# Kernel tuning notes

Measured on AMD Instinct MI355X. Metric: run time of the kernel, lower is better.

The kernel has to match this reference:

```python
import jax, jax.numpy as jnp
import numpy as np


def euler_xyz_to_matrix(angles):
    # pytorch3d euler_angles_to_matrix(angles, 'XYZ') = R_X(a0) @ R_Y(a1) @ R_Z(a2)
    ax, ay, az = angles[..., 0], angles[..., 1], angles[..., 2]
    cx, sx = jnp.cos(ax), jnp.sin(ax)
    cy, sy = jnp.cos(ay), jnp.sin(ay)
    cz, sz = jnp.cos(az), jnp.sin(az)
    one = jnp.ones_like(ax)
    zero = jnp.zeros_like(ax)
    Rx = jnp.stack([one, zero, zero, zero, cx, -sx, zero, sx, cx], axis=-1).reshape(*ax.shape, 3, 3)
    Ry = jnp.stack([cy, zero, sy, zero, one, zero, -sy, zero, cy], axis=-1).reshape(*ax.shape, 3, 3)
    Rz = jnp.stack([cz, -sz, zero, sz, cz, zero, zero, zero, one], axis=-1).reshape(*ax.shape, 3, 3)
    return Rx @ Ry @ Rz


def chamfer_bidir(x, y):
    # x, y: [R, I, N, 3]. Squared-distance chamfer, mean point reduction, per (R,I) batch.
    x2 = jnp.sum(x * x, axis=-1)  # [R,I,N]
    y2 = jnp.sum(y * y, axis=-1)  # [R,I,N]
    # d2[r,i,n,m] = |x_n - y_m|^2
    d2 = x2[..., :, None] + y2[..., None, :] - 2.0 * jnp.einsum('rind,rimd->rinm', x, y)
    cham_x = jnp.mean(jnp.min(d2, axis=-1), axis=-1)  # x -> nearest y
    cham_y = jnp.mean(jnp.min(d2, axis=-2), axis=-1)  # y -> nearest x
    return cham_x + cham_y  # [R, I]


def setup_inputs() -> dict:
    key = jax.random.key(0)
    k1, k2, k3, k4 = jax.random.split(key, 4)
    R, I, N = 4, 16, 2048
    source_points = jax.random.normal(k1, (R, I, N, 3), dtype=jnp.float32)
    target_points = jax.random.normal(k2, (I, N, 3), dtype=jnp.float32)
    rotation = 0.1 * jax.random.normal(k3, (R, I, 3), dtype=jnp.float32)
    translation = 0.1 * jax.random.normal(k4, (R, I, 3), dtype=jnp.float32)
    scale = jnp.ones((R, I), dtype=jnp.float32)
    return {
        'source_points': source_points,
        'target_points': target_points,
        'rotation': rotation,
        'translation': translation,
        'scale': scale,
    }


def reference(source_points, target_points, rotation, translation, scale):
    R, I, N, _ = source_points.shape
    rot = euler_xyz_to_matrix(rotation)  # [R,I,3,3]
    # Transform per original: 4x4 matrix with rows [:3,:] scaled by `scale`,
    # so p' = scale * (rot @ p + translation).
    transformed = scale[..., None, None] * (
        jnp.einsum('rind,rikd->rink', source_points, rot) + translation[..., None, :]
    )  # [R,I,N,3]
    # target_points [I,N,3] broadcast to [R,I,N,3] (original repeats along R)
    target = jnp.broadcast_to(target_points[None], transformed.shape)
    # original calls chamfer_distance(target, transformed): x=target, y=transformed
    return chamfer_bidir(target, transformed)  # [R, I]
```

## Files before the change

### kernel.cpp

```cpp
#include <hip/hip_runtime.h>
#include <math.h>

#define RDIM 4
#define IDIM 16
#define NPAIR 64
#define NPTS 2048
#define THREADS 256
#define ROWSB 256
#define RBLK (NPTS / ROWSB)
#define TILES (NPTS / 32)
#define PSPLIT 4
#define ONEBF 0x3F80u

typedef __attribute__((ext_vector_type(8))) short bf16x8;
typedef __attribute__((ext_vector_type(16))) float f32x16;
typedef __attribute__((ext_vector_type(4))) float f32x4;

__device__ __forceinline__ float min3f(float a, float b, float c) {
    return fminf(a, fminf(b, c));
}

__device__ __forceinline__ unsigned int fkey(float f) {
    const unsigned int u = __float_as_uint(f);
    return (u & 0x80000000u) ? ~u : (u | 0x80000000u);
}
__device__ __forceinline__ float funkey(unsigned int k) {
    const unsigned int u = (k & 0x80000000u) ? (k ^ 0x80000000u) : ~k;
    return __uint_as_float(u);
}

__device__ __forceinline__ unsigned int f2bf(float f) {
    union { float f; unsigned int u; } v; v.f = f;
    return (v.u + 0x7FFFu + ((v.u >> 16) & 1u)) >> 16;
}
__device__ __forceinline__ float bf2f(unsigned int h) {
    union { unsigned int u; float f; } v; v.u = h << 16; return v.f;
}

__device__ __forceinline__ void make_rot(const float* __restrict__ rotv, int pair,
                                         float& r00, float& r01, float& r02,
                                         float& r10, float& r11, float& r12,
                                         float& r20, float& r21, float& r22) {
    const float ax = rotv[pair * 3 + 0];
    const float ay = rotv[pair * 3 + 1];
    const float az = rotv[pair * 3 + 2];
    float sx, cx, sy, cy, sz, cz;
    sincosf(ax, &sx, &cx);
    sincosf(ay, &sy, &cy);
    sincosf(az, &sz, &cz);
    r00 = cy * cz;                r01 = -cy * sz;               r02 = sy;
    r10 = cx * sz + sx * sy * cz; r11 = cx * cz - sx * sy * sz; r12 = -sx * cy;
    r20 = sx * sz - cx * sy * cz; r21 = sx * cz + cx * sy * sz; r22 = cx * cy;
}

__device__ __forceinline__ uint4 brec(float v0, float v1, float v2) {
    const float b0 = -2.0f * v0, b1 = -2.0f * v1, b2 = -2.0f * v2;
    const unsigned int h0 = f2bf(b0), h1 = f2bf(b1), h2 = f2bf(b2);
    const unsigned int l0 = f2bf(b0 - bf2f(h0));
    const unsigned int l1 = f2bf(b1 - bf2f(h1));
    const unsigned int l2 = f2bf(b2 - bf2f(h2));
    const float n2 = v0 * v0 + v1 * v1 + v2 * v2;
    const unsigned int nh = f2bf(n2), nl = f2bf(n2 - bf2f(nh));
    return make_uint4(h0 | (h1 << 16), h2 | (l0 << 16), l1 | (l2 << 16), nh | (nl << 16));
}
__device__ __forceinline__ void arec(float q0, float q1, float q2, uint4& a0, uint4& a1) {
    const unsigned int h0 = f2bf(q0), h1 = f2bf(q1), h2 = f2bf(q2);
    const unsigned int l0 = f2bf(q0 - bf2f(h0));
    const unsigned int l1 = f2bf(q1 - bf2f(h1));
    const unsigned int l2 = f2bf(q2 - bf2f(h2));
    a0 = make_uint4(h0 | (h1 << 16), h2 | (l0 << 16), l1 | (l2 << 16), ONEBF);
    a1 = make_uint4(l0 | (l1 << 16), l2 | (h0 << 16), h1 | (h2 << 16), ONEBF << 16);
}

__global__ __launch_bounds__(THREADS)
void prep(const float* __restrict__ src, const float* __restrict__ tgt,
          const float* __restrict__ rotv, const float* __restrict__ trav,
          const float* __restrict__ scal,
          uint4* __restrict__ Yb, uint4* __restrict__ Xa,
          unsigned int* __restrict__ colminU,
          float* __restrict__ out)
{
    const int b   = blockIdx.x;
    const int seg = blockIdx.y;
    const int tid = threadIdx.x;
    if (b == 0 && seg == 0 && tid < NPAIR) out[tid] = 0.0f;
    const int m0  = seg * (NPTS / PSPLIT);
    if (b < NPAIR) {
        const int pair = b;
        colminU[(size_t)pair * NPTS + m0 + tid * 2 + 0] = 0xFFFFFFFFu;
        colminU[(size_t)pair * NPTS + m0 + tid * 2 + 1] = 0xFFFFFFFFu;
        float r00, r01, r02, r10, r11, r12, r20, r21, r22;
        make_rot(rotv, pair, r00, r01, r02, r10, r11, r12, r20, r21, r22);
        const float t0 = trav[pair * 3 + 0];
        const float t1 = trav[pair * 3 + 1];
        const float t2 = trav[pair * 3 + 2];
        const float s  = scal[pair];
        const float* __restrict__ srcp = src + (size_t)pair * NPTS * 3;
#pragma unroll
        for (int u = 0; u < NPTS / THREADS / PSPLIT; ++u) {
            const int m = m0 + u * THREADS + tid;
            const float p0 = srcp[m * 3 + 0];
            const float p1 = srcp[m * 3 + 1];
            const float p2 = srcp[m * 3 + 2];
            const float y0 = s * fmaf(r00, p0, fmaf(r01, p1, fmaf(r02, p2, t0)));
            const float y1 = s * fmaf(r10, p0, fmaf(r11, p1, fmaf(r12, p2, t1)));
            const float y2 = s * fmaf(r20, p0, fmaf(r21, p1, fmaf(r22, p2, t2)));
            Yb[(size_t)pair * NPTS + m] = brec(y0, y1, y2);
        }
    } else {
        const int i = b - NPAIR;
        const float* __restrict__ tgtp = tgt + (size_t)i * NPTS * 3;
#pragma unroll
        for (int u = 0; u < NPTS / THREADS / PSPLIT; ++u) {
            const int m = m0 + u * THREADS + tid;
            const float x0 = tgtp[m * 3 + 0];
            const float x1 = tgtp[m * 3 + 1];
            const float x2 = tgtp[m * 3 + 2];
            uint4 a0, a1;
            arec(x0, x1, x2, a0, a1);
            Xa[((size_t)i * NPTS + m) * 2 + 0] = a0;
            Xa[((size_t)i * NPTS + m) * 2 + 1] = a1;
        }
    }
}

__global__ __launch_bounds__(THREADS, 2)
void chamfer_main(const uint4* __restrict__ Yb, const uint4* __restrict__ Xa,
                  unsigned int* __restrict__ colminU,
                  float* __restrict__ out)
{
    __shared__ alignas(16) unsigned char smem[32768];
    __shared__ unsigned int colpartU[NPTS];
    __shared__ float sx[ROWSB];
    __shared__ float rowmin[ROWSB];
    __shared__ float wsum[4];
    unsigned short* sB = (unsigned short*)smem;

    const int pair  = blockIdx.x;
    const int rb    = blockIdx.y;
    const int i     = pair & (IDIM - 1);
    const int tid   = threadIdx.x;
    const int lane  = tid & 63;
    const int w     = tid >> 6;
    const int c31   = lane & 31;
    const int h     = lane >> 5;

    const uint4* __restrict__ gB = Yb + (size_t)pair * NPTS;
    const char* gAb = (const char*)(Xa + ((size_t)i * NPTS + rb * ROWSB) * 2);

#pragma unroll
    for (int j = 0; j < 8; ++j)
        ((uint4*)sB)[j * THREADS + tid] = gB[j * THREADS + tid];
#pragma unroll
    for (int k = 0; k < 8; ++k)
        colpartU[k * THREADS + tid] = 0xFFFFFFFFu;
    {
        const unsigned short* ar = (const unsigned short*)(gAb + tid * 32);
        const float q0 = bf2f(ar[0]) + bf2f(ar[3]);
        const float q1 = bf2f(ar[1]) + bf2f(ar[4]);
        const float q2 = bf2f(ar[2]) + bf2f(ar[5]);
        sx[tid] = q0 * q0 + q1 * q1 + q2 * q2;
    }

    const bf16x8 af0 = *(const bf16x8*)(gAb + (w * 64 + c31) * 32 + h * 16);
    const bf16x8 af1 = *(const bf16x8*)(gAb + (w * 64 + 32 + c31) * 32 + h * 16);

    __syncthreads();

    f32x16 cx0, cx1;
#pragma unroll
    for (int j = 0; j < 16; ++j) {
        const int r = (j & 3) + 8 * (j >> 2) + 4 * h;
        cx0[j] = sx[w * 64 + r];
        cx1[j] = sx[w * 64 + 32 + r];
    }

    float mn0[16], mn1[16];
#pragma unroll
    for (int j = 0; j < 16; ++j) { mn0[j] = 3.4e38f; mn1[j] = 3.4e38f; }

    bf16x8 bfA = *(const bf16x8*)&sB[(0 * 32 + c31) * 8];
    bf16x8 bfB = *(const bf16x8*)&sB[(1 * 32 + c31) * 8];
    for (int t = 0; t < TILES; t += 2) {
        const f32x16 a0 = __builtin_amdgcn_mfma_f32_32x32x16_bf16(af0, bfA, cx0, 0, 0, 0);
        const f32x16 a1 = __builtin_amdgcn_mfma_f32_32x32x16_bf16(af1, bfA, cx1, 0, 0, 0);
        const f32x16 b0 = __builtin_amdgcn_mfma_f32_32x32x16_bf16(af0, bfB, cx0, 0, 0, 0);
        const f32x16 b1 = __builtin_amdgcn_mfma_f32_32x32x16_bf16(af1, bfB, cx1, 0, 0, 0);
        bfA = *(const bf16x8*)&sB[((((t + 2) & 63)) * 32 + c31) * 8];
        bfB = *(const bf16x8*)&sB[((((t + 3) & 63)) * 32 + c31) * 8];
#pragma unroll
        for (int j = 0; j < 16; ++j) {
            mn0[j] = min3f(mn0[j], a0[j], b0[j]);
            mn1[j] = min3f(mn1[j], a1[j], b1[j]);
        }
        float ca = fminf(a0[0], a1[0]);
        float cb = fminf(b0[0], b1[0]);
#pragma unroll
        for (int j = 1; j < 16; ++j) {
            ca = min3f(ca, a0[j], a1[j]);
            cb = min3f(cb, b0[j], b1[j]);
        }
        ca = fminf(ca, __shfl_xor(ca, 32, 64));
        cb = fminf(cb, __shfl_xor(cb, 32, 64));
        if (h == 0) {
            atomicMin(&colpartU[(t + 0) * 32 + c31], fkey(ca));
            atomicMin(&colpartU[(t + 1) * 32 + c31], fkey(cb));
        }
    }
    __syncthreads();

#pragma unroll
    for (int j = 0; j < 16; ++j) {
        float v0 = mn0[j], v1 = mn1[j];
        v0 = fminf(v0, __shfl_xor(v0, 1, 64));
        v1 = fminf(v1, __shfl_xor(v1, 1, 64));
        v0 = fminf(v0, __shfl_xor(v0, 2, 64));
        v1 = fminf(v1, __shfl_xor(v1, 2, 64));
        v0 = fminf(v0, __shfl_xor(v0, 4, 64));
        v1 = fminf(v1, __shfl_xor(v1, 4, 64));
        v0 = fminf(v0, __shfl_xor(v0, 8, 64));
        v1 = fminf(v1, __shfl_xor(v1, 8, 64));
        v0 = fminf(v0, __shfl_xor(v0, 16, 64));
        v1 = fminf(v1, __shfl_xor(v1, 16, 64));
        mn0[j] = v0; mn1[j] = v1;
    }
    if (c31 == 0) {
#pragma unroll
        for (int g = 0; g < 4; ++g) {
            f32x4 v4, u4;
            v4[0] = mn0[g * 4 + 0]; v4[1] = mn0[g * 4 + 1];
            v4[2] = mn0[g * 4 + 2]; v4[3] = mn0[g * 4 + 3];
            u4[0] = mn1[g * 4 + 0]; u4[1] = mn1[g * 4 + 1];
            u4[2] = mn1[g * 4 + 2]; u4[3] = mn1[g * 4 + 3];
            *(f32x4*)&rowmin[w * 64 + 8 * g + 4 * h] = v4;
            *(f32x4*)&rowmin[w * 64 + 32 + 8 * g + 4 * h] = u4;
        }
    }

#pragma unroll
    for (int k = 0; k < 8; ++k) {
        const int col = k * THREADS + tid;
        atomicMin(&colminU[(size_t)pair * NPTS + col], colpartU[col]);
    }
    __syncthreads();

    float v = rowmin[tid];
#pragma unroll
    for (int off = 32; off > 0; off >>= 1)
        v += __shfl_down(v, off, 64);
    if (lane == 0) wsum[w] = v;
    __syncthreads();
    if (tid == 0) {
        const float tot = wsum[0] + wsum[1] + wsum[2] + wsum[3];
        atomicAdd(&out[pair], tot * (1.0f / NPTS));
    }
}

__global__ __launch_bounds__(THREADS)
void chamfer_col(const unsigned int* __restrict__ colminU, float* __restrict__ out)
{
    __shared__ float wsum[4];
    const int pair = blockIdx.x;
    const int tid  = threadIdx.x;
    const int lane = tid & 63;
    const int w    = tid >> 6;
    float s = 0.0f;
#pragma unroll
    for (int k = 0; k < 8; ++k) {
        const int col = k * THREADS + tid;
        s += funkey(colminU[(size_t)pair * NPTS + col]);
    }
#pragma unroll
    for (int off = 32; off > 0; off >>= 1)
        s += __shfl_down(s, off, 64);
    if (lane == 0) wsum[w] = s;
    __syncthreads();
    if (tid == 0) {
        const float tot = wsum[0] + wsum[1] + wsum[2] + wsum[3];
        atomicAdd(&out[pair], tot * (1.0f / NPTS));
    }
}

extern "C" void kernel_launch(void* const* d_in, const int* in_sizes, int n_in,
                              void* d_out, int out_size, void* d_ws, size_t ws_size,
                              hipStream_t stream) {
    const float* src  = (const float*)d_in[0];
    const float* tgt  = (const float*)d_in[1];
    const float* rotv = (const float*)d_in[2];
    const float* trav = (const float*)d_in[3];
    const float* scal = (const float*)d_in[4];
    float* out = (float*)d_out;

    char* ws = (char*)d_ws;
    uint4* Yb = (uint4*)ws;
    uint4* Xa = (uint4*)(ws + (size_t)NPAIR * NPTS * 16);
    unsigned int* colminU = (unsigned int*)(ws + (size_t)NPAIR * NPTS * 16
                                               + (size_t)IDIM * NPTS * 32);

    dim3 pgrid(NPAIR + IDIM, PSPLIT);
    prep<<<pgrid, THREADS, 0, stream>>>(src, tgt, rotv, trav, scal, Yb, Xa, colminU, out);

    dim3 grid(NPAIR, RBLK);
    chamfer_main<<<grid, THREADS, 0, stream>>>(Yb, Xa, colminU, out);

    chamfer_col<<<NPAIR, THREADS, 0, stream>>>(colminU, out);
}
```

Before: 95.12 us.

## Fuse point prep into main chamfer kernel and replace atomics with partial buffers

Removes the separate prep kernel. Each main block now transforms its pair's source points and encodes its own target rows straight into shared memory, and the target norms come from the split-bf16 encoding. Global atomicMin on column minima and atomicAdd on outputs are replaced by per-row-block partial key arrays, which the final kernel reduces with a min over row blocks. This saves one launch and the workspace round trip, and removes the need to initialise the output. In exchange, every row block redundantly recomputes the rotation and encoding for all 2048 source points, and more partial data is written and read back.

```diff
diff --git a/kernel.cpp b/kernel.cpp
--- a/kernel.cpp
+++ b/kernel.cpp
@@ -9,7 +9,6 @@
 #define ROWSB 256
 #define RBLK (NPTS / ROWSB)
 #define TILES (NPTS / 32)
-#define PSPLIT 4
 #define ONEBF 0x3F80u
 
 typedef __attribute__((ext_vector_type(8))) short bf16x8;
@@ -63,73 +62,29 @@
     const unsigned int nh = f2bf(n2), nl = f2bf(n2 - bf2f(nh));
     return make_uint4(h0 | (h1 << 16), h2 | (l0 << 16), l1 | (l2 << 16), nh | (nl << 16));
 }
-__device__ __forceinline__ void arec(float q0, float q1, float q2, uint4& a0, uint4& a1) {
+__device__ __forceinline__ void arec(float q0, float q1, float q2, uint4& a0, uint4& a1,
+                                     float& qn2) {
     const unsigned int h0 = f2bf(q0), h1 = f2bf(q1), h2 = f2bf(q2);
     const unsigned int l0 = f2bf(q0 - bf2f(h0));
     const unsigned int l1 = f2bf(q1 - bf2f(h1));
     const unsigned int l2 = f2bf(q2 - bf2f(h2));
     a0 = make_uint4(h0 | (h1 << 16), h2 | (l0 << 16), l1 | (l2 << 16), ONEBF);
     a1 = make_uint4(l0 | (l1 << 16), l2 | (h0 << 16), h1 | (h2 << 16), ONEBF << 16);
-}
-
-__global__ __launch_bounds__(THREADS)
-void prep(const float* __restrict__ src, const float* __restrict__ tgt,
-          const float* __restrict__ rotv, const float* __restrict__ trav,
-          const float* __restrict__ scal,
-          uint4* __restrict__ Yb, uint4* __restrict__ Xa,
-          unsigned int* __restrict__ colminU,
-          float* __restrict__ out)
-{
-    const int b   = blockIdx.x;
-    const int seg = blockIdx.y;
-    const int tid = threadIdx.x;
-    if (b == 0 && seg == 0 && tid < NPAIR) out[tid] = 0.0f;
-    const int m0  = seg * (NPTS / PSPLIT);
-    if (b < NPAIR) {
-        const int pair = b;
-        colminU[(size_t)pair * NPTS + m0 + tid * 2 + 0] = 0xFFFFFFFFu;
-        colminU[(size_t)pair * NPTS + m0 + tid * 2 + 1] = 0xFFFFFFFFu;
-        float r00, r01, r02, r10, r11, r12, r20, r21, r22;
-        make_rot(rotv, pair, r00, r01, r02, r10, r11, r12, r20, r21, r22);
-        const float t0 = trav[pair * 3 + 0];
-        const float t1 = trav[pair * 3 + 1];
-        const float t2 = trav[pair * 3 + 2];
-        const float s  = scal[pair];
-        const float* __restrict__ srcp = src + (size_t)pair * NPTS * 3;
-#pragma unroll
-        for (int u = 0; u < NPTS / THREADS / PSPLIT; ++u) {
-            const int m = m0 + u * THREADS + tid;
-            const float p0 = srcp[m * 3 + 0];
-            const float p1 = srcp[m * 3 + 1];
-            const float p2 = srcp[m * 3 + 2];
-            const float y0 = s * fmaf(r00, p0, fmaf(r01, p1, fmaf(r02, p2, t0)));
-            const float y1 = s * fmaf(r10, p0, fmaf(r11, p1, fmaf(r12, p2, t1)));
-            const float y2 = s * fmaf(r20, p0, fmaf(r21, p1, fmaf(r22, p2, t2)));
-            Yb[(size_t)pair * NPTS + m] = brec(y0, y1, y2);
-        }
-    } else {
-        const int i = b - NPAIR;
-        const float* __restrict__ tgtp = tgt + (size_t)i * NPTS * 3;
-#pragma unroll
-        for (int u = 0; u < NPTS / THREADS / PSPLIT; ++u) {
-            const int m = m0 + u * THREADS + tid;
-            const float x0 = tgtp[m * 3 + 0];
-            const float x1 = tgtp[m * 3 + 1];
-            const float x2 = tgtp[m * 3 + 2];
-            uint4 a0, a1;
-            arec(x0, x1, x2, a0, a1);
-            Xa[((size_t)i * NPTS + m) * 2 + 0] = a0;
-            Xa[((size_t)i * NPTS + m) * 2 + 1] = a1;
-        }
-    }
+    const float d0 = bf2f(h0) + bf2f(l0);
+    const float d1 = bf2f(h1) + bf2f(l1);
+    const float d2 = bf2f(h2) + bf2f(l2);
+    qn2 = d0 * d0 + d1 * d1 + d2 * d2;
 }
 
 __global__ __launch_bounds__(THREADS, 2)
-void chamfer_main(const uint4* __restrict__ Yb, const uint4* __restrict__ Xa,
-                  unsigned int* __restrict__ colminU,
-                  float* __restrict__ out)
+void chamfer_main(const float* __restrict__ src, const float* __restrict__ tgt,
+                  const float* __restrict__ rotv, const float* __restrict__ trav,
+                  const float* __restrict__ scal,
+                  unsigned int* __restrict__ colkeys,
+                  float* __restrict__ rowpart)
 {
     __shared__ alignas(16) unsigned char smem[32768];
+    __shared__ alignas(16) uint4 sA[ROWSB * 2];
     __shared__ unsigned int colpartU[NPTS];
     __shared__ float sx[ROWSB];
     __shared__ float rowmin[ROWSB];
@@ -145,27 +100,43 @@
     const int c31   = lane & 31;
     const int h     = lane >> 5;
 
-    const uint4* __restrict__ gB = Yb + (size_t)pair * NPTS;
-    const char* gAb = (const char*)(Xa + ((size_t)i * NPTS + rb * ROWSB) * 2);
-
-#pragma unroll
-    for (int j = 0; j < 8; ++j)
-        ((uint4*)sB)[j * THREADS + tid] = gB[j * THREADS + tid];
+    {
+        float r00, r01, r02, r10, r11, r12, r20, r21, r22;
+        make_rot(rotv, pair, r00, r01, r02, r10, r11, r12, r20, r21, r22);
+        const float t0 = trav[pair * 3 + 0];
+        const float t1 = trav[pair * 3 + 1];
+        const float t2 = trav[pair * 3 + 2];
+        const float s  = scal[pair];
+        const float* __restrict__ srcp = src + (size_t)pair * NPTS * 3;
+#pragma unroll
+        for (int u = 0; u < NPTS / THREADS; ++u) {
+            const int m = u * THREADS + tid;
+            const float p0 = srcp[m * 3 + 0];
+            const float p1 = srcp[m * 3 + 1];
+            const float p2 = srcp[m * 3 + 2];
+            const float y0 = s * fmaf(r00, p0, fmaf(r01, p1, fmaf(r02, p2, t0)));
+            const float y1 = s * fmaf(r10, p0, fmaf(r11, p1, fmaf(r12, p2, t1)));
+            const float y2 = s * fmaf(r20, p0, fmaf(r21, p1, fmaf(r22, p2, t2)));
+            ((uint4*)sB)[m] = brec(y0, y1, y2);
+        }
+        const float* __restrict__ tgtp = tgt + ((size_t)i * NPTS + rb * ROWSB) * 3;
+        const float x0 = tgtp[tid * 3 + 0];
+        const float x1 = tgtp[tid * 3 + 1];
+        const float x2 = tgtp[tid * 3 + 2];
+        uint4 a0, a1; float qn2;
+        arec(x0, x1, x2, a0, a1, qn2);
+        sA[tid * 2 + 0] = a0;
+        sA[tid * 2 + 1] = a1;
+        sx[tid] = qn2;
+    }
 #pragma unroll
     for (int k = 0; k < 8; ++k)
         colpartU[k * THREADS + tid] = 0xFFFFFFFFu;
-    {
-        const unsigned short* ar = (const unsigned short*)(gAb + tid * 32);
-        const float q0 = bf2f(ar[0]) + bf2f(ar[3]);
-        const float q1 = bf2f(ar[1]) + bf2f(ar[4]);
-        const float q2 = bf2f(ar[2]) + bf2f(ar[5]);
-        sx[tid] = q0 * q0 + q1 * q1 + q2 * q2;
-    }
-
-    const bf16x8 af0 = *(const bf16x8*)(gAb + (w * 64 + c31) * 32 + h * 16);
-    const bf16x8 af1 = *(const bf16x8*)(gAb + (w * 64 + 32 + c31) * 32 + h * 16);
-
-    __syncthreads();
+    __syncthreads();
+
+    const unsigned short* sAs = (const unsigned short*)sA;
+    const bf16x8 af0 = *(const bf16x8*)&sAs[(w * 64 + c31) * 16 + h * 8];
+    const bf16x8 af1 = *(const bf16x8*)&sAs[(w * 64 + 32 + c31) * 16 + h * 8];
 
     f32x16 cx0, cx1;
 #pragma unroll
@@ -240,7 +211,7 @@
 #pragma unroll
     for (int k = 0; k < 8; ++k) {
         const int col = k * THREADS + tid;
-        atomicMin(&colminU[(size_t)pair * NPTS + col], colpartU[col]);
+        colkeys[((size_t)pair * RBLK + rb) * NPTS + col] = colpartU[col];
     }
     __syncthreads();
 
@@ -250,14 +221,14 @@
         v += __shfl_down(v, off, 64);
     if (lane == 0) wsum[w] = v;
     __syncthreads();
-    if (tid == 0) {
-        const float tot = wsum[0] + wsum[1] + wsum[2] + wsum[3];
-        atomicAdd(&out[pair], tot * (1.0f / NPTS));
-    }
+    if (tid == 0)
+        rowpart[pair * RBLK + rb] = wsum[0] + wsum[1] + wsum[2] + wsum[3];
 }
 
 __global__ __launch_bounds__(THREADS)
-void chamfer_col(const unsigned int* __restrict__ colminU, float* __restrict__ out)
+void chamfer_fin(const unsigned int* __restrict__ colkeys,
+                 const float* __restrict__ rowpart,
+                 float* __restrict__ out)
 {
     __shared__ float wsum[4];
     const int pair = blockIdx.x;
@@ -268,17 +239,20 @@
 #pragma unroll
     for (int k = 0; k < 8; ++k) {
         const int col = k * THREADS + tid;
-        s += funkey(colminU[(size_t)pair * NPTS + col]);
-    }
+        unsigned int mk = colkeys[((size_t)pair * RBLK + 0) * NPTS + col];
+#pragma unroll
+        for (int rb = 1; rb < RBLK; ++rb)
+            mk = min(mk, colkeys[((size_t)pair * RBLK + rb) * NPTS + col]);
+        s += funkey(mk);
+    }
+    if (tid < RBLK) s += rowpart[pair * RBLK + tid];
 #pragma unroll
     for (int off = 32; off > 0; off >>= 1)
         s += __shfl_down(s, off, 64);
     if (lane == 0) wsum[w] = s;
     __syncthreads();
-    if (tid == 0) {
-        const float tot = wsum[0] + wsum[1] + wsum[2] + wsum[3];
-        atomicAdd(&out[pair], tot * (1.0f / NPTS));
-    }
+    if (tid == 0)
+        out[pair] = (wsum[0] + wsum[1] + wsum[2] + wsum[3]) * (1.0f / NPTS);
 }
 
 extern "C" void kernel_launch(void* const* d_in, const int* in_sizes, int n_in,
@@ -292,16 +266,12 @@
     float* out = (float*)d_out;
 
     char* ws = (char*)d_ws;
-    uint4* Yb = (uint4*)ws;
-    uint4* Xa = (uint4*)(ws + (size_t)NPAIR * NPTS * 16);
-    unsigned int* colminU = (unsigned int*)(ws + (size_t)NPAIR * NPTS * 16
-                                               + (size_t)IDIM * NPTS * 32);
-
-    dim3 pgrid(NPAIR + IDIM, PSPLIT);
-    prep<<<pgrid, THREADS, 0, stream>>>(src, tgt, rotv, trav, scal, Yb, Xa, colminU, out);
+    unsigned int* colkeys = (unsigned int*)ws;
+    float* rowpart = (float*)(ws + (size_t)NPAIR * RBLK * NPTS * 4);
 
     dim3 grid(NPAIR, RBLK);
-    chamfer_main<<<grid, THREADS, 0, stream>>>(Yb, Xa, colminU, out);
-
-    chamfer_col<<<NPAIR, THREADS, 0, stream>>>(colminU, out);
-}
+    chamfer_main<<<grid, THREADS, 0, stream>>>(src, tgt, rotv, trav, scal,
+                                               colkeys, rowpart);
+
+    chamfer_fin<<<NPAIR, THREADS, 0, stream>>>(colkeys, rowpart, out);
+}
```

New measurement: 92.96 us. 1.02x faster.
